# Kernel tuning notes

Hardware: AMD Instinct MI355X
Metric: run time of the kernel (lower is better)

Reference implementation:

```python
import jax, jax.numpy as jnp
import numpy as np

D = 2048
H = 16
HD = D // H  # 128


def setup_inputs() -> dict:
    key = jax.random.key(0)
    k1, k2, k3 = jax.random.split(key, 3)
    x = jax.random.normal(k1, (2, 2048, D), dtype=jnp.float32)
    # nn.Linear(d, 3d, bias=False): weight [3d, d]; y = x @ W.T
    w_qkv = jax.random.normal(k2, (3 * D, D), dtype=jnp.float32) * (1.0 / np.sqrt(D))
    w_o = jax.random.normal(k3, (D, D), dtype=jnp.float32) * (1.0 / np.sqrt(D))
    return {"x": x, "w_qkv": w_qkv, "w_o": w_o}


def reference(x, w_qkv, w_o):
    B, T, _ = x.shape
    qkv = jnp.einsum('btd,ed->bte', x, w_qkv)  # [B,T,3D]
    q, k, v = jnp.split(qkv, 3, axis=-1)
    # [B,T,D] -> [B,H,T,hd]
    q = q.reshape(B, T, H, HD).transpose(0, 2, 1, 3)
    k = k.reshape(B, T, H, HD).transpose(0, 2, 1, 3)
    v = v.reshape(B, T, H, HD).transpose(0, 2, 1, 3)
    att = jnp.einsum('bhtd,bhsd->bhts', q, k) / np.sqrt(HD).astype(np.float32)
    att = jax.nn.softmax(att, axis=-1)
    y = jnp.einsum('bhts,bhsd->bhtd', att, v)
    y = y.transpose(0, 2, 1, 3).reshape(B, T, D)
    return jnp.einsum('btd,ed->bte', y, w_o)
```

## Files before the change

### kernel.cpp

```cpp
#include <hip/hip_runtime.h>
#include <hip/hip_bf16.h>
#include <math.h>

typedef __bf16 bf16_t;
typedef __attribute__((ext_vector_type(8))) __bf16 bx8;
typedef __attribute__((ext_vector_type(4))) __bf16 bx4;
typedef __attribute__((ext_vector_type(4))) short sx4;
typedef __attribute__((ext_vector_type(4))) float fx4;

#define DEV __device__ __forceinline__

DEV void async_copy16(void* lds, const void* g) {
    __builtin_amdgcn_global_load_lds(
        (const __attribute__((address_space(1))) unsigned int*)g,
        (__attribute__((address_space(3))) unsigned int*)lds, 16, 0, 0);
}

DEV fx4 mfma16(bx4 a, bx4 b, fx4 c) {
#if __has_builtin(__builtin_amdgcn_mfma_f32_16x16x16bf16_1k)
    return __builtin_amdgcn_mfma_f32_16x16x16bf16_1k(
        __builtin_bit_cast(sx4, a), __builtin_bit_cast(sx4, b), c, 0, 0, 0);
#elif __has_builtin(__builtin_amdgcn_mfma_f32_16x16x16_bf16)
    return __builtin_amdgcn_mfma_f32_16x16x16_bf16(a, b, c, 0, 0, 0);
#else
    asm("v_mfma_f32_16x16x16_bf16 %0, %1, %2, %0" : "+v"(c) : "v"(a), "v"(b));
    return c;
#endif
}

__global__ void __launch_bounds__(256) cvt_bf16(const float* __restrict__ in,
                                                bf16_t* __restrict__ out, int n) {
    int i = (blockIdx.x * 256 + threadIdx.x) * 4;
    if (i + 3 < n) {
        float4 v = *(const float4*)(in + i);
        bx4 o = { (__bf16)v.x, (__bf16)v.y, (__bf16)v.z, (__bf16)v.w };
        *(bx4*)(out + i) = o;
    }
}

template <bool BF16_OUT>
__global__ void __launch_bounds__(256, 2) gemm_bt(const bf16_t* __restrict__ A,
                                                  const bf16_t* __restrict__ B,
                                                  void* __restrict__ C,
                                                  int M, int N, int K, float scale0) {
    __shared__ bf16_t As[2 * 4096];
    __shared__ bf16_t Bs[2 * 4096];
    const int tid = threadIdx.x;
    const int w = tid >> 6, lane = tid & 63;
    const int ln = lane & 15, quad = lane >> 4;
    const int m0 = blockIdx.y * 128, n0 = blockIdx.x * 128;
    const int wm = (w >> 1) * 64, wn = (w & 1) * 64;
    const float scale = (n0 < 2048) ? scale0 : 1.0f;

    fx4 acc[4][4];
#pragma unroll
    for (int i = 0; i < 4; ++i)
#pragma unroll
        for (int j = 0; j < 4; ++j) acc[i][j] = (fx4){0.f, 0.f, 0.f, 0.f};

    for (int k0 = 0; k0 < K; k0 += 64) {
#pragma unroll
        for (int call = 0; call < 4; ++call) {
            int c = w * 256 + call * 64 + lane;
            int p = c >> 9, row = (c >> 2) & 127, piece = c & 3;
            async_copy16(As + (size_t)(w * 256 + call * 64) * 8,
                         A + (size_t)(m0 + row) * K + k0 + p * 32 + piece * 8);
            async_copy16(Bs + (size_t)(w * 256 + call * 64) * 8,
                         B + (size_t)(n0 + row) * K + k0 + p * 32 + piece * 8);
        }
        __syncthreads();

#pragma unroll
        for (int kk = 0; kk < 2; ++kk) {
            bx8 af[4], bf[4];
#pragma unroll
            for (int i = 0; i < 4; ++i)
                af[i] = *(const bx8*)(As + (size_t)kk * 4096 + (wm + i * 16 + ln) * 32 + quad * 8);
#pragma unroll
            for (int j = 0; j < 4; ++j)
                bf[j] = *(const bx8*)(Bs + (size_t)kk * 4096 + (wn + j * 16 + ln) * 32 + quad * 8);
#pragma unroll
            for (int i = 0; i < 4; ++i)
#pragma unroll
                for (int j = 0; j < 4; ++j)
                    acc[i][j] = __builtin_amdgcn_mfma_f32_16x16x32_bf16(af[i], bf[j], acc[i][j], 0, 0, 0);
        }
        __syncthreads();
    }

#pragma unroll
    for (int i = 0; i < 4; ++i) {
        int mrow = m0 + wm + i * 16 + quad * 4;
#pragma unroll
        for (int j = 0; j < 4; ++j) {
            int ncol = n0 + wn + j * 16 + ln;
#pragma unroll
            for (int r = 0; r < 4; ++r) {
                if (BF16_OUT)
                    ((bf16_t*)C)[(size_t)(mrow + r) * N + ncol] = (__bf16)(acc[i][j][r] * scale);
                else
                    ((float*)C)[(size_t)(mrow + r) * N + ncol] = acc[i][j][r];
            }
        }
    }
}

__global__ void __launch_bounds__(256) vpack(const bf16_t* __restrict__ qkv,
                                             bf16_t* __restrict__ vp) {
    int g = blockIdx.x * 256 + threadIdx.x;
    int bh = g >> 15;
    int rem = g & 32767;
    int q4 = rem >> 6;
    int c  = rem & 63;
    int b = bh >> 4, h = bh & 15;
    const bf16_t* src = qkv + (size_t)(b * 2048 + q4 * 4) * 6144 + 4096 + h * 128 + c * 2;
    unsigned u0 = *(const unsigned*)(src);
    unsigned u1 = *(const unsigned*)(src + 6144);
    unsigned u2 = *(const unsigned*)(src + 12288);
    unsigned u3 = *(const unsigned*)(src + 18432);
    uint4 outv;
    outv.x = (u0 & 0xffffu) | (u1 << 16);
    outv.y = (u2 & 0xffffu) | (u3 << 16);
    outv.z = (u0 >> 16) | (u1 & 0xffff0000u);
    outv.w = (u2 >> 16) | (u3 & 0xffff0000u);
    *(uint4*)(vp + (size_t)g * 8) = outv;
}

__global__ void __launch_bounds__(256, 2) attn(const bf16_t* __restrict__ qkv,
                                               const bf16_t* __restrict__ vp,
                                               bf16_t* __restrict__ y) {
    __shared__ bf16_t Ks[128 * 128];
    __shared__ bf16_t Vs[16384];
    const int tid = threadIdx.x;
    const int w = tid >> 6, lane = tid & 63;
    const int ln = lane & 15, quad = lane >> 4;
    const int lin = blockIdx.x;
    const int slot = lin >> 3;
    const int bh = (lin & 7) + ((slot >> 4) << 3);
    const int qt = slot & 15;
    const int b = bh >> 4, h = bh & 15;

    const bf16_t* Qb = qkv + (size_t)(b * 2048 + qt * 128) * 6144 + h * 128;
    const bf16_t* Kb = qkv + (size_t)(b * 2048) * 6144 + 2048 + h * 128;
    const bf16_t* VPb = vp + (size_t)bh * 262144;

    bx8 qf[2][4];
#pragma unroll
    for (int i = 0; i < 2; ++i)
#pragma unroll
        for (int kk = 0; kk < 4; ++kk)
            qf[i][kk] = *(const bx8*)(Qb + (size_t)(w * 32 + i * 16 + ln) * 6144 + kk * 32 + quad * 8);

    const __bf16 one = (__bf16)1.0f;
    const bx4 ones4 = { one, one, one, one };

    fx4 o[2][8];
#pragma unroll
    for (int i = 0; i < 2; ++i)
#pragma unroll
        for (int j = 0; j < 8; ++j) o[i][j] = (fx4){0.f, 0.f, 0.f, 0.f};
    fx4 lsum[2];
#pragma unroll
    for (int i = 0; i < 2; ++i) lsum[i] = (fx4){0.f, 0.f, 0.f, 0.f};

    for (int kt = 0; kt < 16; ++kt) {
#pragma unroll
        for (int call = 0; call < 8; ++call) {
            int cp = call * 64 + lane;
            int row = cp >> 2, piece = cp & 3;
            async_copy16(Ks + (size_t)w * 4096 + call * 512,
                         Kb + (size_t)(kt * 128 + row) * 6144 + w * 32 + piece * 8);
            async_copy16(Vs + (size_t)w * 4096 + call * 512,
                         VPb + (size_t)kt * 16384 + (w * 8 + call) * 512 + lane * 8);
        }
        __syncthreads();

#pragma unroll
        for (int q = 0; q < 4; ++q) {
            fx4 st[2][2];
#pragma unroll
            for (int i = 0; i < 2; ++i)
#pragma unroll
                for (int jj = 0; jj < 2; ++jj) st[i][jj] = (fx4){0.f, 0.f, 0.f, 0.f};
#pragma unroll
            for (int kk = 0; kk < 4; ++kk) {
                bx8 kf0 = *(const bx8*)(Ks + (size_t)kk * 4096 + ((2 * q) * 16 + ln) * 32 + quad * 8);
                bx8 kf1 = *(const bx8*)(Ks + (size_t)kk * 4096 + ((2 * q + 1) * 16 + ln) * 32 + quad * 8);
#pragma unroll
                for (int i = 0; i < 2; ++i) {
                    st[i][0] = __builtin_amdgcn_mfma_f32_16x16x32_bf16(kf0, qf[i][kk], st[i][0], 0, 0, 0);
                    st[i][1] = __builtin_amdgcn_mfma_f32_16x16x32_bf16(kf1, qf[i][kk], st[i][1], 0, 0, 0);
                }
            }

            bx4 pa[2][2];
#pragma unroll
            for (int i = 0; i < 2; ++i)
#pragma unroll
                for (int jj = 0; jj < 2; ++jj) {
                    bx4 t = { (__bf16)exp2f(st[i][jj][0]), (__bf16)exp2f(st[i][jj][1]),
                              (__bf16)exp2f(st[i][jj][2]), (__bf16)exp2f(st[i][jj][3]) };
                    pa[i][jj] = t;
                }

#pragma unroll
            for (int jj = 0; jj < 2; ++jj) {
                const int kt8 = 2 * q + jj;
                bx4 vf[8];
#pragma unroll
                for (int j = 0; j < 8; ++j)
                    vf[j] = *(const bx4*)(Vs + (size_t)(kt8 * 4 + quad) * 512 + (j * 16 + ln) * 4);
#pragma unroll
                for (int i = 0; i < 2; ++i) {
#pragma unroll
                    for (int j = 0; j < 8; ++j)
                        o[i][j] = mfma16(pa[i][jj], vf[j], o[i][j]);
                    lsum[i] = mfma16(pa[i][jj], ones4, lsum[i]);
                }
            }
        }
        __syncthreads();
    }

#pragma unroll
    for (int i = 0; i < 2; ++i)
#pragma unroll
        for (int r = 0; r < 4; ++r) {
            float rl = 1.0f / lsum[i][r];
#pragma unroll
            for (int j = 0; j < 8; ++j) {
                int t = qt * 128 + w * 32 + i * 16 + quad * 4 + r;
                int col = h * 128 + j * 16 + ln;
                y[(size_t)(b * 2048 + t) * 2048 + col] = (__bf16)(o[i][j][r] * rl);
            }
        }
}

extern "C" void kernel_launch(void* const* d_in, const int* in_sizes, int n_in,
                              void* d_out, int out_size, void* d_ws, size_t ws_size,
                              hipStream_t stream) {
    const float* x    = (const float*)d_in[0];
    const float* wqkv = (const float*)d_in[1];
    const float* wo   = (const float*)d_in[2];
    float* out = (float*)d_out;
    char* ws = (char*)d_ws;
    const float CEXP = 0.08838834764831845f * 1.44269504088896340f;

    bf16_t* Xb  = (bf16_t*)(ws);
    bf16_t* Wqb = (bf16_t*)(ws + (size_t)(16u << 20));
    bf16_t* Wob = (bf16_t*)(ws + (size_t)(40u << 20));
    bf16_t* QKV = (bf16_t*)(ws + (size_t)(48u << 20));
    bf16_t* VP  = (bf16_t*)(ws + (size_t)(96u << 20));
    bf16_t* Y   = Xb;

    cvt_bf16<<<8388608 / 1024, 256, 0, stream>>>(x, Xb, 8388608);
    cvt_bf16<<<12582912 / 1024, 256, 0, stream>>>(wqkv, Wqb, 12582912);
    cvt_bf16<<<4194304 / 1024, 256, 0, stream>>>(wo, Wob, 4194304);

    gemm_bt<true><<<dim3(48, 32), 256, 0, stream>>>(Xb, Wqb, QKV, 4096, 6144, 2048, CEXP);
    vpack<<<4096, 256, 0, stream>>>(QKV, VP);
    attn<<<dim3(512), 256, 0, stream>>>(QKV, VP, Y);
    gemm_bt<false><<<dim3(16, 32), 256, 0, stream>>>(Y, Wob, out, 4096, 2048, 2048, 1.0f);
}
```

Baseline: 387.3 us.

## Fuse V packing into QKV GEMM epilogue and merge conversion kernels

The QKV GEMM epilogue now writes V tiles directly into the packed 4-key-interleaved layout the attention kernel expects, which removes the separate vpack kernel and its re-read of V from QKV. The three fp32-to-bf16 conversion launches are merged into one kernel that picks its source by index range. This cuts two launches and an extra global pass over V. The V epilogue writes 8-byte vectors where it used to do scalar stores, but V is no longer written to the QKV buffer itself.

```diff
diff --git a/kernel.cpp b/kernel.cpp
--- a/kernel.cpp
+++ b/kernel.cpp
@@ -28,20 +28,29 @@
 #endif
 }
 
-__global__ void __launch_bounds__(256) cvt_bf16(const float* __restrict__ in,
-                                                bf16_t* __restrict__ out, int n) {
+__global__ void __launch_bounds__(256) cvt_all(const float* __restrict__ x,
+                                               const float* __restrict__ wq,
+                                               const float* __restrict__ wo,
+                                               bf16_t* __restrict__ xb,
+                                               bf16_t* __restrict__ wqb,
+                                               bf16_t* __restrict__ wob) {
     int i = (blockIdx.x * 256 + threadIdx.x) * 4;
-    if (i + 3 < n) {
-        float4 v = *(const float4*)(in + i);
-        bx4 o = { (__bf16)v.x, (__bf16)v.y, (__bf16)v.z, (__bf16)v.w };
-        *(bx4*)(out + i) = o;
-    }
+    const float* in;
+    bf16_t* out;
+    int k;
+    if (i < 8388608) { in = x; out = xb; k = i; }
+    else if (i < 8388608 + 12582912) { in = wq; out = wqb; k = i - 8388608; }
+    else { in = wo; out = wob; k = i - (8388608 + 12582912); }
+    float4 v = *(const float4*)(in + k);
+    bx4 o = { (__bf16)v.x, (__bf16)v.y, (__bf16)v.z, (__bf16)v.w };
+    *(bx4*)(out + k) = o;
 }
 
 template <bool BF16_OUT>
 __global__ void __launch_bounds__(256, 2) gemm_bt(const bf16_t* __restrict__ A,
                                                   const bf16_t* __restrict__ B,
                                                   void* __restrict__ C,
+                                                  bf16_t* __restrict__ VP,
                                                   int M, int N, int K, float scale0) {
     __shared__ bf16_t As[2 * 4096];
     __shared__ bf16_t Bs[2 * 4096];
@@ -88,42 +97,39 @@
         __syncthreads();
     }
 
-#pragma unroll
-    for (int i = 0; i < 4; ++i) {
-        int mrow = m0 + wm + i * 16 + quad * 4;
-#pragma unroll
-        for (int j = 0; j < 4; ++j) {
-            int ncol = n0 + wn + j * 16 + ln;
-#pragma unroll
-            for (int r = 0; r < 4; ++r) {
-                if (BF16_OUT)
-                    ((bf16_t*)C)[(size_t)(mrow + r) * N + ncol] = (__bf16)(acc[i][j][r] * scale);
-                else
-                    ((float*)C)[(size_t)(mrow + r) * N + ncol] = acc[i][j][r];
+    if (VP != nullptr && n0 >= 4096) {
+        const int h = (n0 - 4096) >> 7;
+        const int bidx = m0 >> 11;
+        bf16_t* vpb = VP + (size_t)(bidx * 16 + h) * 262144;
+        const int key_base = (m0 & 2047) + wm;
+#pragma unroll
+        for (int i = 0; i < 4; ++i) {
+            int key = key_base + i * 16 + quad * 4;
+#pragma unroll
+            for (int j = 0; j < 4; ++j) {
+                int hd = wn + j * 16 + ln;
+                bx4 v = { (__bf16)acc[i][j][0], (__bf16)acc[i][j][1],
+                          (__bf16)acc[i][j][2], (__bf16)acc[i][j][3] };
+                *(bx4*)(vpb + (size_t)(key >> 2) * 512 + hd * 4) = v;
+            }
+        }
+    } else {
+#pragma unroll
+        for (int i = 0; i < 4; ++i) {
+            int mrow = m0 + wm + i * 16 + quad * 4;
+#pragma unroll
+            for (int j = 0; j < 4; ++j) {
+                int ncol = n0 + wn + j * 16 + ln;
+#pragma unroll
+                for (int r = 0; r < 4; ++r) {
+                    if (BF16_OUT)
+                        ((bf16_t*)C)[(size_t)(mrow + r) * N + ncol] = (__bf16)(acc[i][j][r] * scale);
+                    else
+                        ((float*)C)[(size_t)(mrow + r) * N + ncol] = acc[i][j][r];
+                }
             }
         }
     }
-}
-
-__global__ void __launch_bounds__(256) vpack(const bf16_t* __restrict__ qkv,
-                                             bf16_t* __restrict__ vp) {
-    int g = blockIdx.x * 256 + threadIdx.x;
-    int bh = g >> 15;
-    int rem = g & 32767;
-    int q4 = rem >> 6;
-    int c  = rem & 63;
-    int b = bh >> 4, h = bh & 15;
-    const bf16_t* src = qkv + (size_t)(b * 2048 + q4 * 4) * 6144 + 4096 + h * 128 + c * 2;
-    unsigned u0 = *(const unsigned*)(src);
-    unsigned u1 = *(const unsigned*)(src + 6144);
-    unsigned u2 = *(const unsigned*)(src + 12288);
-    unsigned u3 = *(const unsigned*)(src + 18432);
-    uint4 outv;
-    outv.x = (u0 & 0xffffu) | (u1 << 16);
-    outv.y = (u2 & 0xffffu) | (u3 << 16);
-    outv.z = (u0 >> 16) | (u1 & 0xffff0000u);
-    outv.w = (u2 >> 16) | (u3 & 0xffff0000u);
-    *(uint4*)(vp + (size_t)g * 8) = outv;
 }
 
 __global__ void __launch_bounds__(256, 2) attn(const bf16_t* __restrict__ qkv,
@@ -253,12 +259,9 @@
     bf16_t* VP  = (bf16_t*)(ws + (size_t)(96u << 20));
     bf16_t* Y   = Xb;
 
-    cvt_bf16<<<8388608 / 1024, 256, 0, stream>>>(x, Xb, 8388608);
-    cvt_bf16<<<12582912 / 1024, 256, 0, stream>>>(wqkv, Wqb, 12582912);
-    cvt_bf16<<<4194304 / 1024, 256, 0, stream>>>(wo, Wob, 4194304);
-
-    gemm_bt<true><<<dim3(48, 32), 256, 0, stream>>>(Xb, Wqb, QKV, 4096, 6144, 2048, CEXP);
-    vpack<<<4096, 256, 0, stream>>>(QKV, VP);
+    cvt_all<<<24576, 256, 0, stream>>>(x, wqkv, wo, Xb, Wqb, Wob);
+
+    gemm_bt<true><<<dim3(48, 32), 256, 0, stream>>>(Xb, Wqb, QKV, VP, 4096, 6144, 2048, CEXP);
     attn<<<dim3(512), 256, 0, stream>>>(QKV, VP, Y);
-    gemm_bt<false><<<dim3(16, 32), 256, 0, stream>>>(Y, Wob, out, 4096, 2048, 2048, 1.0f);
-}
+    gemm_bt<false><<<dim3(16, 32), 256, 0, stream>>>(Y, Wob, out, nullptr, 4096, 2048, 2048, 1.0f);
+}
```

New measurement: 368.3 us. 4.9% less time.
